# Performance work log

Measured on AMD Instinct MI355X. Metric: run time of the kernel, lower is better.

Reference implementation:

```python
import jax, jax.numpy as jnp
import numpy as np

H = 8          # num_heads
DK = 64        # head dim (head_size // num_heads)
SPARSITY = 0.5 # pre-softmax random drop probability
DROPOUT = 0.1  # post-softmax dropout probability


def setup_inputs() -> dict:
    key = jax.random.key(0)
    ks = jax.random.split(key, 12)
    B, S, D = 4, 2048, 512
    mk = lambda k, shp, scale=1.0: (jax.random.normal(k, shp, dtype=jnp.float32) * scale)
    return {
        "query": mk(ks[0], (B, S, D)),
        "key": mk(ks[1], (B, S, D)),
        "value": mk(ks[2], (B, S, D)),
        "Wq": mk(ks[3], (D, D), 0.04),
        "bq": mk(ks[4], (D,), 0.02),
        "Wk": mk(ks[5], (D, D), 0.04),
        "bk": mk(ks[6], (D,), 0.02),
        "Wv": mk(ks[7], (D, D), 0.04),
        "bv": mk(ks[8], (D,), 0.02),
        "Wo": mk(ks[9], (D, D), 0.04),
        "bo": mk(ks[10], (D,), 0.02),
    }


def _split_heads(x, B):
    # [B, S, H*DK] -> [B, H, S, DK]
    return x.reshape(B, -1, H, DK).transpose(0, 2, 1, 3)


def reference(query, key, value, Wq, bq, Wk, bk, Wv, bv, Wo, bo):
    B, S, D = query.shape
    # q/k/v projections (torch Linear: x @ W.T + b)
    q = _split_heads(query @ Wq.T + bq, B)   # [B, H, S, DK]
    k = _split_heads(key @ Wk.T + bk, B)
    v = _split_heads(value @ Wv.T + bv, B)

    scores = jnp.einsum("bhqd,bhkd->bhqk", q, k) / jnp.sqrt(jnp.float32(DK))

    # random pre-softmax sparsity mask: keep where U(0,1) > sparsity
    mkey = jax.random.fold_in(jax.random.key(42), 1)
    keep_sparse = jax.random.uniform(mkey, scores.shape) > SPARSITY
    scores = jnp.where(keep_sparse, scores, -jnp.inf)

    p_attn = jax.nn.softmax(scores, axis=-1)

    # dropout on attention probs, inverted scaling as in torch
    dkey = jax.random.fold_in(jax.random.key(42), 2)
    keep_drop = jax.random.uniform(dkey, p_attn.shape) >= DROPOUT
    p_attn = jnp.where(keep_drop, p_attn / (1.0 - DROPOUT), 0.0)

    x = jnp.einsum("bhqk,bhkd->bhqd", p_attn, v)        # [B, H, S, DK]
    x = x.transpose(0, 2, 1, 3).reshape(B, S, H * DK)    # [B, S, D]
    return x @ Wo.T + bo
```

## Files before the change

### kernel.cpp

```cpp
#include <hip/hip_runtime.h>
#include <stdint.h>

#define BATCH  4
#define SQ     2048
#define DMODEL 512
#define NH     8
#define DK     64

typedef __attribute__((ext_vector_type(8))) short short8;
typedef __attribute__((ext_vector_type(4))) float f32x4;

struct TFK { uint32_t a, b; };
constexpr uint32_t rotl_ce(uint32_t x, int d) {
  return (x << d) | (x >> (32 - d));
}
constexpr TFK tf_ce(uint32_t k0, uint32_t k1, uint32_t x0, uint32_t x1) {
  const uint32_t ks[3] = {k0, k1, k0 ^ k1 ^ 0x1BD11BDAu};
  const int rot[2][4] = {{13, 15, 26, 6}, {17, 29, 16, 24}};
  x0 += k0; x1 += k1;
  for (int c = 0; c < 5; ++c) {
    for (int j = 0; j < 4; ++j) {
      x0 += x1; x1 = rotl_ce(x1, rot[c & 1][j]); x1 ^= x0;
    }
    x0 += ks[(c + 1) % 3];
    x1 += ks[(c + 2) % 3] + (uint32_t)(c + 1);
  }
  return TFK{x0, x1};
}
constexpr TFK SPK = tf_ce(0u, 42u, 0u, 1u);
constexpr TFK DPK = tf_ce(0u, 42u, 0u, 2u);

#define SP_THR 0x80000200u
#define DP_THR 0x1999A200u

struct TfArgs {
  uint32_t sp[8];
  uint32_t dp[8];
  uint32_t sp_thr, dp_thr;
};

__device__ __forceinline__ void tf_round(uint32_t &x0, uint32_t &x1, int d) {
  x0 += x1;
  x1 = __builtin_amdgcn_alignbit(x1, x1, 32 - d);
  x1 ^= x0;
}
__device__ __forceinline__ void tf_grp(uint32_t &x0, uint32_t &x1,
                                       uint32_t injx1, uint32_t injx0, int d0,
                                       int d1, int d2, int d3) {
  x1 += injx1;
  x0 = x0 + injx0 + x1;
  x1 = __builtin_amdgcn_alignbit(x1, x1, 32 - d0);
  x1 ^= x0;
  tf_round(x0, x1, d1);
  tf_round(x0, x1, d2);
  tf_round(x0, x1, d3);
}
__device__ __forceinline__ uint32_t tf_rt(const uint32_t *__restrict__ c,
                                          uint32_t ctr) {
  uint32_t x1 = c[1] + ctr;
  uint32_t x0 = c[0] + x1;
  x1 = __builtin_amdgcn_alignbit(x1, x1, 19);
  x1 ^= x0;
  tf_round(x0, x1, 15);
  tf_round(x0, x1, 26);
  tf_round(x0, x1, 6);
  tf_grp(x0, x1, c[2], c[1], 17, 29, 16, 24);
  tf_grp(x0, x1, c[3], c[7], 13, 15, 26, 6);
  tf_grp(x0, x1, c[4], c[0], 17, 29, 16, 24);
  tf_grp(x0, x1, c[5], c[1], 13, 15, 26, 6);
  return (x0 + c[7]) ^ (x1 + c[6]);
}

__device__ __forceinline__ ushort f2bf_rne(float f) {
  uint32_t u = __float_as_uint(f);
  return (ushort)((u + 0x7fffu + ((u >> 16) & 1u)) >> 16);
}
__device__ __forceinline__ float bf2f(ushort h) {
  return __uint_as_float((uint32_t)h << 16);
}
__device__ __forceinline__ float exp_scaled(float s) {
#if __has_builtin(__builtin_amdgcn_exp2f)
  return __builtin_amdgcn_exp2f(s * 0.18033688011112042f);
#else
  return __expf(s * 0.125f);
#endif
}

__device__ __forceinline__ void split4(const float *__restrict__ src,
                                       ushort *__restrict__ dh,
                                       ushort *__restrict__ dl, size_t base) {
  float4 x = *(const float4 *)(src + base);
  uint32_t h[4], lo[4];
#pragma unroll
  for (int i = 0; i < 4; ++i) {
    float xi = ((const float *)&x)[i];
    ushort hh = f2bf_rne(xi);
    h[i] = hh;
    lo[i] = f2bf_rne(xi - bf2f(hh));
  }
  uint2 ph, pl;
  ph.x = h[0] | (h[1] << 16);  ph.y = h[2] | (h[3] << 16);
  pl.x = lo[0] | (lo[1] << 16); pl.y = lo[2] | (lo[3] << 16);
  *(uint2 *)(dh + base) = ph;
  *(uint2 *)(dl + base) = pl;
}

__global__ __launch_bounds__(256) void split_inputs_k(
    const float *__restrict__ q, const float *__restrict__ k,
    const float *__restrict__ v, ushort *__restrict__ qh,
    ushort *__restrict__ ql, ushort *__restrict__ kh, ushort *__restrict__ kl,
    ushort *__restrict__ vh, ushort *__restrict__ vl) {
  const float *src = blockIdx.y == 0 ? q : (blockIdx.y == 1 ? k : v);
  ushort *dh = blockIdx.y == 0 ? qh : (blockIdx.y == 1 ? kh : vh);
  ushort *dl = blockIdx.y == 0 ? ql : (blockIdx.y == 1 ? kl : vl);
  const size_t base = ((size_t)blockIdx.x * 256 + threadIdx.x) * 4;
  split4(src, dh, dl, base);
}

__global__ __launch_bounds__(256) void split_w_k(
    const float *__restrict__ w0, const float *__restrict__ w1,
    const float *__restrict__ w2, const float *__restrict__ w3,
    ushort *__restrict__ h0, ushort *__restrict__ l0, ushort *__restrict__ h1,
    ushort *__restrict__ l1, ushort *__restrict__ h2, ushort *__restrict__ l2,
    ushort *__restrict__ h3, ushort *__restrict__ l3) {
  const int y = blockIdx.y;
  const float *src = y == 0 ? w0 : (y == 1 ? w1 : (y == 2 ? w2 : w3));
  ushort *dh = y == 0 ? h0 : (y == 1 ? h1 : (y == 2 ? h2 : h3));
  ushort *dl = y == 0 ? l0 : (y == 1 ? l1 : (y == 2 ? l2 : l3));
  const size_t base = ((size_t)blockIdx.x * 256 + threadIdx.x) * 4;
  split4(src, dh, dl, base);
}

template <int MODE>
__global__ __launch_bounds__(256) void proj_mfma(
    const ushort *__restrict__ Ah, const ushort *__restrict__ Al,
    const ushort *__restrict__ Bh, const ushort *__restrict__ Bl,
    const float *__restrict__ bias, void *__restrict__ Yv) {
  __shared__ ushort Tt[MODE == 2 ? 128 * 72 : 1];
  const int tid = threadIdx.x;
  const int w = tid >> 6, l = tid & 63;
  const int lr = l & 15, lq = l >> 4;
  const int am = blockIdx.y * 128 + w * 32;
  const int bn = blockIdx.x * 64;
  f32x4 acc[2][4];
#pragma unroll
  for (int i = 0; i < 2; ++i)
#pragma unroll
    for (int j = 0; j < 4; ++j) acc[i][j] = (f32x4){0.f, 0.f, 0.f, 0.f};

#pragma unroll 2
  for (int k0 = 0; k0 < DMODEL; k0 += 32) {
    short8 ah[2], al[2], bh[4], bl[4];
#pragma unroll
    for (int mf = 0; mf < 2; ++mf) {
      const size_t off = (size_t)(am + mf * 16 + lr) * DMODEL + k0 + lq * 8;
      ah[mf] = *(const short8 *)(Ah + off);
      al[mf] = *(const short8 *)(Al + off);
    }
#pragma unroll
    for (int nf = 0; nf < 4; ++nf) {
      const size_t off = (size_t)(bn + nf * 16 + lr) * DMODEL + k0 + lq * 8;
      bh[nf] = *(const short8 *)(Bh + off);
      bl[nf] = *(const short8 *)(Bl + off);
    }
#pragma unroll
    for (int mf = 0; mf < 2; ++mf)
#pragma unroll
      for (int nf = 0; nf < 4; ++nf) {
        acc[mf][nf] = __builtin_amdgcn_mfma_f32_16x16x32_bf16(
            ah[mf], bh[nf], acc[mf][nf], 0, 0, 0);
        acc[mf][nf] = __builtin_amdgcn_mfma_f32_16x16x32_bf16(
            ah[mf], bl[nf], acc[mf][nf], 0, 0, 0);
        acc[mf][nf] = __builtin_amdgcn_mfma_f32_16x16x32_bf16(
            al[mf], bh[nf], acc[mf][nf], 0, 0, 0);
      }
  }

  if (MODE == 2) {
#pragma unroll
    for (int mf = 0; mf < 2; ++mf)
#pragma unroll
      for (int nf = 0; nf < 4; ++nf) {
        const int gn2 = am + mf * 16 + lq * 4;
#pragma unroll
        for (int r = 0; r < 4; ++r) {
          const int featl = (w * 32 + mf * 16 + lq * 4 + r);
          Tt[featl * 72 + nf * 16 + lr] =
              f2bf_rne(acc[mf][nf][r] + bias[gn2 + r]);
        }
      }
    __syncthreads();
    ushort *Y = (ushort *)Yv;
    const int feat = tid >> 1, half = tid & 1;
    const int gfeat = blockIdx.y * 128 + feat;
    const int bcol = bn >> 11, scol = (bn & 2047) + half * 32;
    ushort *dst = Y + ((size_t)(bcol * DMODEL + gfeat)) * SQ + scol;
    const ushort *srcp = &Tt[feat * 72 + half * 32];
#pragma unroll
    for (int j = 0; j < 4; ++j)
      *(uint4 *)(dst + j * 8) = *(const uint4 *)(srcp + j * 8);
    return;
  }

#pragma unroll
  for (int mf = 0; mf < 2; ++mf)
#pragma unroll
    for (int nf = 0; nf < 4; ++nf) {
      const int gn = bn + nf * 16 + lr;
      const float bb = bias[gn];
      if (MODE == 0) {
        float *Y = (float *)Yv;
#pragma unroll
        for (int r = 0; r < 4; ++r) {
          const int gm = am + mf * 16 + lq * 4 + r;
          Y[(size_t)gm * DMODEL + gn] = acc[mf][nf][r] + bb;
        }
      } else {
        ushort *Y = (ushort *)Yv;
#pragma unroll
        for (int r = 0; r < 4; ++r) {
          const int gm = am + mf * 16 + lq * 4 + r;
          Y[(size_t)gm * DMODEL + gn] = f2bf_rne(acc[mf][nf][r] + bb);
        }
      }
    }
}

__global__ __launch_bounds__(256, 2) void attn_mfma(
    const ushort *__restrict__ qp, const ushort *__restrict__ kp,
    const ushort *__restrict__ vpt, ushort *__restrict__ xah,
    ushort *__restrict__ xal, TfArgs ta) {
  __shared__ __align__(16) uint8_t lds[40960];
  const int b = blockIdx.z, h = blockIdx.y;
  const int qb = blockIdx.x * 64;
  const int tid = threadIdx.x;
  const int w = tid >> 6, l = tid & 63;
  const int lr = l & 15, lq = l >> 4;
  uint8_t *Ps = lds + 32768 + w * 2048;
  const int bh = b * NH + h;

  short8 qf[2];
  {
    const int qrow = qb + w * 16 + lr;
    const ushort *qrowp = qp + ((size_t)(b * SQ + qrow)) * DMODEL + h * DK;
    qf[0] = *(const short8 *)(qrowp + lq * 8);
    qf[1] = *(const short8 *)(qrowp + 32 + lq * 8);
  }
  f32x4 o[4];
  f32x4 lacc;
#pragma unroll
  for (int nd = 0; nd < 4; ++nd) o[nd] = (f32x4){0.f, 0.f, 0.f, 0.f};
  lacc = (f32x4){0.f, 0.f, 0.f, 0.f};

  uint32_t rowflat[4];
#pragma unroll
  for (int r = 0; r < 4; ++r)
    rowflat[r] = ((uint32_t)(bh * SQ + qb + w * 16 + lq * 4 + r)) << 11;

  const int srow = tid >> 2;
  const int sc0 = (tid & 3) * 2;
  const int ssw = (srow & 7) << 4;
  const ushort *kbase =
      kp + ((size_t)(b * SQ) + srow) * DMODEL + h * DK + sc0 * 8;
  const ushort *vbase = vpt + ((size_t)(bh * DK + srow)) * SQ + sc0 * 8;
  const int la0 = (srow * 128 + sc0 * 16) ^ ssw;
  const int la1 = (srow * 128 + (sc0 + 1) * 16) ^ ssw;

  uint4 kr0, kr1, vr0, vr1;
#define ISSUE(kv_)                                            \
  {                                                           \
    const ushort *ks_ = kbase + (size_t)(kv_)*DMODEL;         \
    kr0 = *(const uint4 *)ks_;                                \
    kr1 = *(const uint4 *)(ks_ + 8);                          \
    const ushort *vs_ = vbase + (kv_);                        \
    vr0 = *(const uint4 *)vs_;                                \
    vr1 = *(const uint4 *)(vs_ + 8);                          \
  }
#define STORE(buf_)                                           \
  {                                                           \
    uint8_t *Kb_ = lds + (buf_)*8192;                         \
    uint8_t *Vb_ = lds + 16384 + (buf_)*8192;                 \
    *(uint4 *)(Kb_ + la0) = kr0;                              \
    *(uint4 *)(Kb_ + la1) = kr1;                              \
    *(uint4 *)(Vb_ + la0) = vr0;                              \
    *(uint4 *)(Vb_ + la1) = vr1;                              \
  }

  ISSUE(0)
  STORE(0)
  __syncthreads();

  for (int kv = 0; kv < SQ; kv += 64) {
    const int cur = (kv >> 6) & 1;
    uint8_t *Ks = lds + cur * 8192;
    uint8_t *Vt = lds + 16384 + cur * 8192;
    const bool more = (kv + 64) < SQ;
    if (more) ISSUE(kv + 64)

    f32x4 s[4];
#pragma unroll
    for (int ni = 0; ni < 4; ++ni) s[ni] = (f32x4){0.f, 0.f, 0.f, 0.f};
#pragma unroll
    for (int ni = 0; ni < 4; ++ni) {
      const int krow = ni * 16 + lr;
      const int sw = (krow & 7) << 4;
#pragma unroll
      for (int kf = 0; kf < 2; ++kf) {
        short8 kb =
            *(const short8 *)(Ks + ((krow * 128 + kf * 64 + lq * 16) ^ sw));
        s[ni] =
            __builtin_amdgcn_mfma_f32_16x16x32_bf16(qf[kf], kb, s[ni], 0, 0, 0);
      }
    }

    const uint32_t colbase = (uint32_t)(kv + lr);
#pragma unroll
    for (int ni = 0; ni < 4; ++ni) {
#pragma unroll
      for (int r = 0; r < 4; ++r) {
        const uint32_t ctr = rowflat[r] + colbase + (uint32_t)(ni * 16);
        const bool keep_s = tf_rt(ta.sp, ctr) >= ta.sp_thr;
        const bool keep_d = tf_rt(ta.dp, ctr) >= ta.dp_thr;
        float e = exp_scaled(s[ni][r]);
        float p = keep_s ? e : 0.0f;
        lacc[r] += p;
        float pd = keep_d ? p * (1.0f / 0.9f) : 0.0f;
        const int prow = lq * 4 + r;
        *(ushort *)(Ps +
                    ((prow * 128 + (ni * 16 + lr) * 2) ^ ((prow & 7) << 4))) =
            f2bf_rne(pd);
      }
    }

#pragma unroll
    for (int kf = 0; kf < 2; ++kf) {
      short8 pa = *(const short8 *)(Ps + ((lr * 128 + kf * 64 + lq * 16) ^
                                          ((lr & 7) << 4)));
#pragma unroll
      for (int nd = 0; nd < 4; ++nd) {
        const int vrow = nd * 16 + lr;
        short8 vb = *(const short8 *)(Vt + ((vrow * 128 + kf * 64 + lq * 16) ^
                                            ((vrow & 7) << 4)));
        o[nd] = __builtin_amdgcn_mfma_f32_16x16x32_bf16(pa, vb, o[nd], 0, 0, 0);
      }
    }

    if (more) STORE(cur ^ 1)
    __syncthreads();
  }
#undef ISSUE
#undef STORE

  float inv[4];
#pragma unroll
  for (int r = 0; r < 4; ++r) {
    float t = lacc[r];
    t += __shfl_xor(t, 1);
    t += __shfl_xor(t, 2);
    t += __shfl_xor(t, 4);
    t += __shfl_xor(t, 8);
    inv[r] = 1.0f / t;
  }
#pragma unroll
  for (int nd = 0; nd < 4; ++nd)
#pragma unroll
    for (int r = 0; r < 4; ++r) {
      const int qrow = qb + w * 16 + lq * 4 + r;
      const size_t idx =
          ((size_t)(b * SQ + qrow)) * DMODEL + h * DK + nd * 16 + lr;
      const float val = o[nd][r] * inv[r];
      const ushort hh = f2bf_rne(val);
      xah[idx] = hh;
      xal[idx] = f2bf_rne(val - bf2f(hh));
    }
}

extern "C" void kernel_launch(void *const *d_in, const int *in_sizes, int n_in,
                              void *d_out, int out_size, void *d_ws,
                              size_t ws_size, hipStream_t stream) {
  (void)in_sizes; (void)n_in; (void)out_size;
  const float *query = (const float *)d_in[0];
  const float *key_  = (const float *)d_in[1];
  const float *value = (const float *)d_in[2];
  const float *Wq = (const float *)d_in[3];
  const float *bq = (const float *)d_in[4];
  const float *Wk = (const float *)d_in[5];
  const float *bk = (const float *)d_in[6];
  const float *Wv = (const float *)d_in[7];
  const float *bv = (const float *)d_in[8];
  const float *Wo = (const float *)d_in[9];
  const float *bo = (const float *)d_in[10];
  float *out = (float *)d_out;

  const size_t MB = (size_t)1 << 20;
  if (ws_size < 92 * MB) return;

  char *ws = (char *)d_ws;
  ushort *qih = (ushort *)(ws);
  ushort *qil = (ushort *)(ws + 8 * MB);
  ushort *kih = (ushort *)(ws + 16 * MB);
  ushort *kil = (ushort *)(ws + 24 * MB);
  ushort *vih = (ushort *)(ws + 32 * MB);
  ushort *vil = (ushort *)(ws + 40 * MB);
  ushort *Wqh = (ushort *)(ws + 48 * MB);
  ushort *Wql = (ushort *)(ws + 48 * MB + 512 * 1024);
  ushort *Wkh = (ushort *)(ws + 49 * MB);
  ushort *Wkl = (ushort *)(ws + 49 * MB + 512 * 1024);
  ushort *Wvh = (ushort *)(ws + 50 * MB);
  ushort *Wvl = (ushort *)(ws + 50 * MB + 512 * 1024);
  ushort *Woh = (ushort *)(ws + 51 * MB);
  ushort *Wol = (ushort *)(ws + 51 * MB + 512 * 1024);
  ushort *qp  = (ushort *)(ws + 52 * MB);
  ushort *kp  = (ushort *)(ws + 60 * MB);
  ushort *vpt = (ushort *)(ws + 68 * MB);
  ushort *xah = (ushort *)(ws + 76 * MB);
  ushort *xal = (ushort *)(ws + 84 * MB);

  constexpr uint32_t KS2s = SPK.a ^ SPK.b ^ 0x1BD11BDAu;
  constexpr uint32_t KS2d = DPK.a ^ DPK.b ^ 0x1BD11BDAu;
  TfArgs ta = {
      {SPK.a, SPK.b, KS2s + 1u, SPK.a + 2u, SPK.b + 3u, KS2s + 4u, SPK.a + 5u,
       KS2s},
      {DPK.a, DPK.b, KS2d + 1u, DPK.a + 2u, DPK.b + 3u, KS2d + 4u, DPK.a + 5u,
       KS2d},
      SP_THR, DP_THR};

  split_inputs_k<<<dim3(4096, 3), 256, 0, stream>>>(query, key_, value, qih,
                                                    qil, kih, kil, vih, vil);
  split_w_k<<<dim3(256, 4), 256, 0, stream>>>(Wq, Wk, Wv, Wo, Wqh, Wql, Wkh,
                                              Wkl, Wvh, Wvl, Woh, Wol);

  proj_mfma<1><<<dim3(8, 64), 256, 0, stream>>>(qih, qil, Wqh, Wql, bq, qp);
  proj_mfma<1><<<dim3(8, 64), 256, 0, stream>>>(kih, kil, Wkh, Wkl, bk, kp);
  proj_mfma<2><<<dim3(128, 4), 256, 0, stream>>>(Wvh, Wvl, vih, vil, bv, vpt);

  attn_mfma<<<dim3(SQ / 64, NH, BATCH), 256, 0, stream>>>(qp, kp, vpt, xah,
                                                          xal, ta);

  proj_mfma<0><<<dim3(8, 64), 256, 0, stream>>>(xah, xal, Woh, Wol, bo, out);
}
```

Measured before the change: 715.5 us.

## Precompute part of dropout/sparsity bitmasks in earlier memory-bound kernels

Moves Threefry mask generation for the last portion of attention rows (rows at or past ROW_CUT) into the split and projection kernels. Each thread there packs 32 keep bits for both masks into words stored in the workspace. Attention blocks past the cut then read two uint2 words per row instead of running the RNG per element. The goal is to hide ALU-heavy RNG work inside kernels bound by memory or MFMA. The cost is extra workspace, extra work in the earlier kernels, and an uneven split of work across attention blocks.

```diff
diff --git a/kernel.cpp b/kernel.cpp
--- a/kernel.cpp
+++ b/kernel.cpp
@@ -6,6 +6,10 @@
 #define DMODEL 512
 #define NH     8
 #define DK     64
+
+#define ROW_CUT   57344u
+#define W0        3670016u
+#define NPAIR     524288u
 
 typedef __attribute__((ext_vector_type(8))) short short8;
 typedef __attribute__((ext_vector_type(4))) float f32x4;
@@ -71,6 +75,21 @@
   return (x0 + c[7]) ^ (x1 + c[6]);
 }
 
+__device__ __forceinline__ void gen_mask_pair(uint32_t pairidx,
+                                              const TfArgs &ta,
+                                              uint32_t *__restrict__ spw,
+                                              uint32_t *__restrict__ dpw) {
+  const uint32_t base = (W0 + pairidx) << 5;
+  uint32_t sw = 0u, dw = 0u;
+#pragma unroll 4
+  for (uint32_t t = 0; t < 32; ++t) {
+    sw |= (tf_rt(ta.sp, base + t) >= ta.sp_thr ? 1u : 0u) << t;
+    dw |= (tf_rt(ta.dp, base + t) >= ta.dp_thr ? 1u : 0u) << t;
+  }
+  spw[pairidx] = sw;
+  dpw[pairidx] = dw;
+}
+
 __device__ __forceinline__ ushort f2bf_rne(float f) {
   uint32_t u = __float_as_uint(f);
   return (ushort)((u + 0x7fffu + ((u >> 16) & 1u)) >> 16);
@@ -109,12 +128,16 @@
     const float *__restrict__ q, const float *__restrict__ k,
     const float *__restrict__ v, ushort *__restrict__ qh,
     ushort *__restrict__ ql, ushort *__restrict__ kh, ushort *__restrict__ kl,
-    ushort *__restrict__ vh, ushort *__restrict__ vl) {
+    ushort *__restrict__ vh, ushort *__restrict__ vl,
+    uint32_t *__restrict__ spw, uint32_t *__restrict__ dpw, TfArgs ta) {
   const float *src = blockIdx.y == 0 ? q : (blockIdx.y == 1 ? k : v);
   ushort *dh = blockIdx.y == 0 ? qh : (blockIdx.y == 1 ? kh : vh);
   ushort *dl = blockIdx.y == 0 ? ql : (blockIdx.y == 1 ? kl : vl);
   const size_t base = ((size_t)blockIdx.x * 256 + threadIdx.x) * 4;
   split4(src, dh, dl, base);
+  const uint32_t flat =
+      (blockIdx.y * 4096u + blockIdx.x) * 256u + threadIdx.x;
+  if (flat < 131072u) gen_mask_pair(flat, ta, spw, dpw);
 }
 
 __global__ __launch_bounds__(256) void split_w_k(
@@ -122,20 +145,25 @@
     const float *__restrict__ w2, const float *__restrict__ w3,
     ushort *__restrict__ h0, ushort *__restrict__ l0, ushort *__restrict__ h1,
     ushort *__restrict__ l1, ushort *__restrict__ h2, ushort *__restrict__ l2,
-    ushort *__restrict__ h3, ushort *__restrict__ l3) {
+    ushort *__restrict__ h3, ushort *__restrict__ l3,
+    uint32_t *__restrict__ spw, uint32_t *__restrict__ dpw, TfArgs ta) {
   const int y = blockIdx.y;
   const float *src = y == 0 ? w0 : (y == 1 ? w1 : (y == 2 ? w2 : w3));
   ushort *dh = y == 0 ? h0 : (y == 1 ? h1 : (y == 2 ? h2 : h3));
   ushort *dl = y == 0 ? l0 : (y == 1 ? l1 : (y == 2 ? l2 : l3));
   const size_t base = ((size_t)blockIdx.x * 256 + threadIdx.x) * 4;
   split4(src, dh, dl, base);
+  const uint32_t flat = (blockIdx.y * 256u + blockIdx.x) * 256u + threadIdx.x;
+  if (flat < 32768u) gen_mask_pair(131072u + flat, ta, spw, dpw);
 }
 
 template <int MODE>
 __global__ __launch_bounds__(256) void proj_mfma(
     const ushort *__restrict__ Ah, const ushort *__restrict__ Al,
     const ushort *__restrict__ Bh, const ushort *__restrict__ Bl,
-    const float *__restrict__ bias, void *__restrict__ Yv) {
+    const float *__restrict__ bias, void *__restrict__ Yv,
+    uint32_t mbase, uint32_t mcount, uint32_t *__restrict__ spw,
+    uint32_t *__restrict__ dpw, TfArgs ta) {
   __shared__ ushort Tt[MODE == 2 ? 128 * 72 : 1];
   const int tid = threadIdx.x;
   const int w = tid >> 6, l = tid & 63;
@@ -199,37 +227,43 @@
 #pragma unroll
     for (int j = 0; j < 4; ++j)
       *(uint4 *)(dst + j * 8) = *(const uint4 *)(srcp + j * 8);
-    return;
-  }
-
-#pragma unroll
-  for (int mf = 0; mf < 2; ++mf)
-#pragma unroll
-    for (int nf = 0; nf < 4; ++nf) {
-      const int gn = bn + nf * 16 + lr;
-      const float bb = bias[gn];
-      if (MODE == 0) {
-        float *Y = (float *)Yv;
-#pragma unroll
-        for (int r = 0; r < 4; ++r) {
-          const int gm = am + mf * 16 + lq * 4 + r;
-          Y[(size_t)gm * DMODEL + gn] = acc[mf][nf][r] + bb;
+  } else {
+#pragma unroll
+    for (int mf = 0; mf < 2; ++mf)
+#pragma unroll
+      for (int nf = 0; nf < 4; ++nf) {
+        const int gn = bn + nf * 16 + lr;
+        const float bb = bias[gn];
+        if (MODE == 0) {
+          float *Y = (float *)Yv;
+#pragma unroll
+          for (int r = 0; r < 4; ++r) {
+            const int gm = am + mf * 16 + lq * 4 + r;
+            Y[(size_t)gm * DMODEL + gn] = acc[mf][nf][r] + bb;
+          }
+        } else {
+          ushort *Y = (ushort *)Yv;
+#pragma unroll
+          for (int r = 0; r < 4; ++r) {
+            const int gm = am + mf * 16 + lq * 4 + r;
+            Y[(size_t)gm * DMODEL + gn] = f2bf_rne(acc[mf][nf][r] + bb);
+          }
         }
-      } else {
-        ushort *Y = (ushort *)Yv;
-#pragma unroll
-        for (int r = 0; r < 4; ++r) {
-          const int gm = am + mf * 16 + lq * 4 + r;
-          Y[(size_t)gm * DMODEL + gn] = f2bf_rne(acc[mf][nf][r] + bb);
-        }
-      }
-    }
+      }
+  }
+
+  if (mcount) {
+    const uint32_t flat =
+        (blockIdx.y * gridDim.x + blockIdx.x) * 256u + threadIdx.x;
+    if (flat < mcount) gen_mask_pair(mbase + flat, ta, spw, dpw);
+  }
 }
 
 __global__ __launch_bounds__(256, 2) void attn_mfma(
     const ushort *__restrict__ qp, const ushort *__restrict__ kp,
     const ushort *__restrict__ vpt, ushort *__restrict__ xah,
-    ushort *__restrict__ xal, TfArgs ta) {
+    ushort *__restrict__ xal, const uint32_t *__restrict__ spw,
+    const uint32_t *__restrict__ dpw, TfArgs ta) {
   __shared__ __align__(16) uint8_t lds[40960];
   const int b = blockIdx.z, h = blockIdx.y;
   const int qb = blockIdx.x * 64;
@@ -238,6 +272,7 @@
   const int lr = l & 15, lq = l >> 4;
   uint8_t *Ps = lds + 32768 + w * 2048;
   const int bh = b * NH + h;
+  const bool use_pre = (uint32_t)(bh * SQ + qb) >= ROW_CUT;
 
   short8 qf[2];
   {
@@ -252,10 +287,13 @@
   for (int nd = 0; nd < 4; ++nd) o[nd] = (f32x4){0.f, 0.f, 0.f, 0.f};
   lacc = (f32x4){0.f, 0.f, 0.f, 0.f};
 
-  uint32_t rowflat[4];
-#pragma unroll
-  for (int r = 0; r < 4; ++r)
-    rowflat[r] = ((uint32_t)(bh * SQ + qb + w * 16 + lq * 4 + r)) << 11;
+  uint32_t rowflat[4], rowcomp[4];
+#pragma unroll
+  for (int r = 0; r < 4; ++r) {
+    const uint32_t rowidx = (uint32_t)(bh * SQ + qb + w * 16 + lq * 4 + r);
+    rowflat[r] = rowidx << 11;
+    rowcomp[r] = (rowidx - ROW_CUT) * 64u;
+  }
 
   const int srow = tid >> 2;
   const int sc0 = (tid & 3) * 2;
@@ -313,22 +351,45 @@
       }
     }
 
-    const uint32_t colbase = (uint32_t)(kv + lr);
-#pragma unroll
-    for (int ni = 0; ni < 4; ++ni) {
+    auto process = [&](int ni, int r, bool keep_s, bool keep_d) {
+      float e = exp_scaled(s[ni][r]);
+      float p = keep_s ? e : 0.0f;
+      lacc[r] += p;
+      float pd = keep_d ? p * (1.0f / 0.9f) : 0.0f;
+      const int prow = lq * 4 + r;
+      *(ushort *)(Ps +
+                  ((prow * 128 + (ni * 16 + lr) * 2) ^ ((prow & 7) << 4))) =
+          f2bf_rne(pd);
+    };
+
+    if (!use_pre) {
+      const uint32_t colbase = (uint32_t)(kv + lr);
+#pragma unroll
+      for (int ni = 0; ni < 4; ++ni) {
+#pragma unroll
+        for (int r = 0; r < 4; ++r) {
+          const uint32_t ctr = rowflat[r] + colbase + (uint32_t)(ni * 16);
+          process(ni, r, tf_rt(ta.sp, ctr) >= ta.sp_thr,
+                  tf_rt(ta.dp, ctr) >= ta.dp_thr);
+        }
+      }
+    } else {
+      uint2 swd[4], dwd[4];
 #pragma unroll
       for (int r = 0; r < 4; ++r) {
-        const uint32_t ctr = rowflat[r] + colbase + (uint32_t)(ni * 16);
-        const bool keep_s = tf_rt(ta.sp, ctr) >= ta.sp_thr;
-        const bool keep_d = tf_rt(ta.dp, ctr) >= ta.dp_thr;
-        float e = exp_scaled(s[ni][r]);
-        float p = keep_s ? e : 0.0f;
-        lacc[r] += p;
-        float pd = keep_d ? p * (1.0f / 0.9f) : 0.0f;
-        const int prow = lq * 4 + r;
-        *(ushort *)(Ps +
-                    ((prow * 128 + (ni * 16 + lr) * 2) ^ ((prow & 7) << 4))) =
-            f2bf_rne(pd);
+        const uint32_t wb = rowcomp[r] + (uint32_t)(kv >> 5);
+        swd[r] = *(const uint2 *)(spw + wb);
+        dwd[r] = *(const uint2 *)(dpw + wb);
+      }
+#pragma unroll
+      for (int ni = 0; ni < 4; ++ni) {
+        const int bpos = (ni & 1) * 16 + lr;
+#pragma unroll
+        for (int r = 0; r < 4; ++r) {
+          const uint32_t sws = (ni < 2) ? swd[r].x : swd[r].y;
+          const uint32_t dws = (ni < 2) ? dwd[r].x : dwd[r].y;
+          process(ni, r, (sws >> bpos) & 1u, (dws >> bpos) & 1u);
+        }
       }
     }
 
@@ -393,7 +454,7 @@
   float *out = (float *)d_out;
 
   const size_t MB = (size_t)1 << 20;
-  if (ws_size < 92 * MB) return;
+  if (ws_size < 96 * MB) return;
 
   char *ws = (char *)d_ws;
   ushort *qih = (ushort *)(ws);
@@ -415,6 +476,8 @@
   ushort *vpt = (ushort *)(ws + 68 * MB);
   ushort *xah = (ushort *)(ws + 76 * MB);
   ushort *xal = (ushort *)(ws + 84 * MB);
+  uint32_t *spw = (uint32_t *)(ws + 92 * MB);
+  uint32_t *dpw = (uint32_t *)(ws + 94 * MB);
 
   constexpr uint32_t KS2s = SPK.a ^ SPK.b ^ 0x1BD11BDAu;
   constexpr uint32_t KS2d = DPK.a ^ DPK.b ^ 0x1BD11BDAu;
@@ -425,17 +488,22 @@
        KS2d},
       SP_THR, DP_THR};
 
-  split_inputs_k<<<dim3(4096, 3), 256, 0, stream>>>(query, key_, value, qih,
-                                                    qil, kih, kil, vih, vil);
+  split_inputs_k<<<dim3(4096, 3), 256, 0, stream>>>(
+      query, key_, value, qih, qil, kih, kil, vih, vil, spw, dpw, ta);
   split_w_k<<<dim3(256, 4), 256, 0, stream>>>(Wq, Wk, Wv, Wo, Wqh, Wql, Wkh,
-                                              Wkl, Wvh, Wvl, Woh, Wol);
-
-  proj_mfma<1><<<dim3(8, 64), 256, 0, stream>>>(qih, qil, Wqh, Wql, bq, qp);
-  proj_mfma<1><<<dim3(8, 64), 256, 0, stream>>>(kih, kil, Wkh, Wkl, bk, kp);
-  proj_mfma<2><<<dim3(128, 4), 256, 0, stream>>>(Wvh, Wvl, vih, vil, bv, vpt);
+                                              Wkl, Wvh, Wvl, Woh, Wol, spw,
+                                              dpw, ta);
+
+  proj_mfma<1><<<dim3(8, 64), 256, 0, stream>>>(qih, qil, Wqh, Wql, bq, qp,
+                                                163840u, 131072u, spw, dpw, ta);
+  proj_mfma<1><<<dim3(8, 64), 256, 0, stream>>>(kih, kil, Wkh, Wkl, bk, kp,
+                                                294912u, 131072u, spw, dpw, ta);
+  proj_mfma<2><<<dim3(128, 4), 256, 0, stream>>>(Wvh, Wvl, vih, vil, bv, vpt,
+                                                 425984u, 98304u, spw, dpw, ta);
 
   attn_mfma<<<dim3(SQ / 64, NH, BATCH), 256, 0, stream>>>(qp, kp, vpt, xah,
-                                                          xal, ta);
-
-  proj_mfma<0><<<dim3(8, 64), 256, 0, stream>>>(xah, xal, Woh, Wol, bo, out);
-}
+                                                          xal, spw, dpw, ta);
+
+  proj_mfma<0><<<dim3(8, 64), 256, 0, stream>>>(xah, xal, Woh, Wol, bo, out, 0u,
+                                                0u, spw, dpw, ta);
+}
```

Result: slower. 784.5 us (+9.6%).

## Fuse fp32-to-bf16 split of query/key into projection GEMM and merge split kernels

Applied to the files above, without the earlier changes.

The Q and K projections now read fp32 activations directly and do the hi/lo bf16 split in registers. This removes the separate split pass and its 16 MB-per-tensor scratch writes and reads. The remaining value and weight splits are merged into one launch, the Q and K projections share one launch, and the output projection uses a new tiling of one 16-row fragment per wave with wider N. The trade-off is that A-side split work is recomputed for each N tile, and the loop is not unrolled, which may reduce latency hiding.

```diff
diff --git a/kernel.cpp b/kernel.cpp
--- a/kernel.cpp
+++ b/kernel.cpp
@@ -105,38 +105,126 @@
   *(uint2 *)(dl + base) = pl;
 }
 
-__global__ __launch_bounds__(256) void split_inputs_k(
+__global__ __launch_bounds__(256) void split_all(
+    const float *__restrict__ value, const float *__restrict__ Wq,
+    const float *__restrict__ Wk, const float *__restrict__ Wv,
+    const float *__restrict__ Wo, ushort *__restrict__ vh,
+    ushort *__restrict__ vl, ushort *__restrict__ Wqh,
+    ushort *__restrict__ Wql, ushort *__restrict__ Wkh,
+    ushort *__restrict__ Wkl, ushort *__restrict__ Wvh,
+    ushort *__restrict__ Wvl, ushort *__restrict__ Woh,
+    ushort *__restrict__ Wol) {
+  const int bid = blockIdx.x;
+  const float *src;
+  ushort *dh, *dl;
+  uint32_t lb;
+  if (bid < 4096) {
+    src = value; dh = vh; dl = vl; lb = bid;
+  } else {
+    const int t = bid - 4096;
+    const int wsel = t >> 8;
+    lb = t & 255;
+    src = wsel == 0 ? Wq : (wsel == 1 ? Wk : (wsel == 2 ? Wv : Wo));
+    dh = wsel == 0 ? Wqh : (wsel == 1 ? Wkh : (wsel == 2 ? Wvh : Woh));
+    dl = wsel == 0 ? Wql : (wsel == 1 ? Wkl : (wsel == 2 ? Wvl : Wol));
+  }
+  const size_t base = ((size_t)lb * 256 + threadIdx.x) * 4;
+  split4(src, dh, dl, base);
+}
+
+template <int NF, bool ASPL, bool FOUT>
+__device__ __forceinline__ void proj_body(
+    const float *__restrict__ Af, const ushort *__restrict__ Ah,
+    const ushort *__restrict__ Al, const ushort *__restrict__ Bh,
+    const ushort *__restrict__ Bl, const float *__restrict__ bias,
+    void *__restrict__ Yv, int am, int bn, int lr, int lq) {
+  f32x4 acc[NF];
+#pragma unroll
+  for (int nf = 0; nf < NF; ++nf) acc[nf] = (f32x4){0.f, 0.f, 0.f, 0.f};
+  const int arow = am + lr;
+
+#pragma unroll 1
+  for (int k0 = 0; k0 < DMODEL; k0 += 32) {
+    short8 ah, al;
+    if (ASPL) {
+      const float *ap = Af + (size_t)arow * DMODEL + k0 + lq * 8;
+      float4 x0 = *(const float4 *)ap;
+      float4 x1 = *(const float4 *)(ap + 4);
+      float xs[8] = {x0.x, x0.y, x0.z, x0.w, x1.x, x1.y, x1.z, x1.w};
+#pragma unroll
+      for (int i = 0; i < 8; ++i) {
+        const ushort hh = f2bf_rne(xs[i]);
+        ((ushort *)&ah)[i] = hh;
+        ((ushort *)&al)[i] = f2bf_rne(xs[i] - bf2f(hh));
+      }
+    } else {
+      const size_t off = (size_t)arow * DMODEL + k0 + lq * 8;
+      ah = *(const short8 *)(Ah + off);
+      al = *(const short8 *)(Al + off);
+    }
+#pragma unroll
+    for (int nf = 0; nf < NF; ++nf) {
+      const size_t off = (size_t)(bn + nf * 16 + lr) * DMODEL + k0 + lq * 8;
+      short8 bh = *(const short8 *)(Bh + off);
+      short8 bl = *(const short8 *)(Bl + off);
+      acc[nf] = __builtin_amdgcn_mfma_f32_16x16x32_bf16(ah, bh, acc[nf], 0, 0, 0);
+      acc[nf] = __builtin_amdgcn_mfma_f32_16x16x32_bf16(ah, bl, acc[nf], 0, 0, 0);
+      acc[nf] = __builtin_amdgcn_mfma_f32_16x16x32_bf16(al, bh, acc[nf], 0, 0, 0);
+    }
+  }
+
+#pragma unroll
+  for (int nf = 0; nf < NF; ++nf) {
+    const int gn = bn + nf * 16 + lr;
+    const float bb = bias[gn];
+#pragma unroll
+    for (int r = 0; r < 4; ++r) {
+      const int gm = am + lq * 4 + r;
+      if (FOUT)
+        ((float *)Yv)[(size_t)gm * DMODEL + gn] = acc[nf][r] + bb;
+      else
+        ((ushort *)Yv)[(size_t)gm * DMODEL + gn] = f2bf_rne(acc[nf][r] + bb);
+    }
+  }
+}
+
+__global__ __launch_bounds__(256) void proj_qk(
     const float *__restrict__ q, const float *__restrict__ k,
-    const float *__restrict__ v, ushort *__restrict__ qh,
-    ushort *__restrict__ ql, ushort *__restrict__ kh, ushort *__restrict__ kl,
-    ushort *__restrict__ vh, ushort *__restrict__ vl) {
-  const float *src = blockIdx.y == 0 ? q : (blockIdx.y == 1 ? k : v);
-  ushort *dh = blockIdx.y == 0 ? qh : (blockIdx.y == 1 ? kh : vh);
-  ushort *dl = blockIdx.y == 0 ? ql : (blockIdx.y == 1 ? kl : vl);
-  const size_t base = ((size_t)blockIdx.x * 256 + threadIdx.x) * 4;
-  split4(src, dh, dl, base);
-}
-
-__global__ __launch_bounds__(256) void split_w_k(
-    const float *__restrict__ w0, const float *__restrict__ w1,
-    const float *__restrict__ w2, const float *__restrict__ w3,
-    ushort *__restrict__ h0, ushort *__restrict__ l0, ushort *__restrict__ h1,
-    ushort *__restrict__ l1, ushort *__restrict__ h2, ushort *__restrict__ l2,
-    ushort *__restrict__ h3, ushort *__restrict__ l3) {
-  const int y = blockIdx.y;
-  const float *src = y == 0 ? w0 : (y == 1 ? w1 : (y == 2 ? w2 : w3));
-  ushort *dh = y == 0 ? h0 : (y == 1 ? h1 : (y == 2 ? h2 : h3));
-  ushort *dl = y == 0 ? l0 : (y == 1 ? l1 : (y == 2 ? l2 : l3));
-  const size_t base = ((size_t)blockIdx.x * 256 + threadIdx.x) * 4;
-  split4(src, dh, dl, base);
-}
-
-template <int MODE>
-__global__ __launch_bounds__(256) void proj_mfma(
+    const ushort *__restrict__ Wqh, const ushort *__restrict__ Wql,
+    const ushort *__restrict__ Wkh, const ushort *__restrict__ Wkl,
+    const float *__restrict__ bq, const float *__restrict__ bk,
+    ushort *__restrict__ qp, ushort *__restrict__ kp) {
+  const int tid = threadIdx.x;
+  const int w = tid >> 6, l = tid & 63;
+  const int lr = l & 15, lq = l >> 4;
+  const int am = blockIdx.y * 64 + w * 16;
+  const int bn = blockIdx.x * 256;
+  if (blockIdx.z == 0)
+    proj_body<16, true, false>(q, nullptr, nullptr, Wqh, Wql, bq, qp, am, bn,
+                               lr, lq);
+  else
+    proj_body<16, true, false>(k, nullptr, nullptr, Wkh, Wkl, bk, kp, am, bn,
+                               lr, lq);
+}
+
+__global__ __launch_bounds__(256) void proj_out(
+    const ushort *__restrict__ xah, const ushort *__restrict__ xal,
+    const ushort *__restrict__ Woh, const ushort *__restrict__ Wol,
+    const float *__restrict__ bo, float *__restrict__ out) {
+  const int tid = threadIdx.x;
+  const int w = tid >> 6, l = tid & 63;
+  const int lr = l & 15, lq = l >> 4;
+  const int am = blockIdx.y * 64 + w * 16;
+  const int bn = blockIdx.x * 128;
+  proj_body<8, false, true>(nullptr, xah, xal, Woh, Wol, bo, out, am, bn, lr,
+                            lq);
+}
+
+__global__ __launch_bounds__(256) void proj_vt(
     const ushort *__restrict__ Ah, const ushort *__restrict__ Al,
     const ushort *__restrict__ Bh, const ushort *__restrict__ Bl,
-    const float *__restrict__ bias, void *__restrict__ Yv) {
-  __shared__ ushort Tt[MODE == 2 ? 128 * 72 : 1];
+    const float *__restrict__ bias, ushort *__restrict__ Y) {
+  __shared__ ushort Tt[128 * 72];
   const int tid = threadIdx.x;
   const int w = tid >> 6, l = tid & 63;
   const int lr = l & 15, lq = l >> 4;
@@ -176,54 +264,27 @@
       }
   }
 
-  if (MODE == 2) {
-#pragma unroll
-    for (int mf = 0; mf < 2; ++mf)
-#pragma unroll
-      for (int nf = 0; nf < 4; ++nf) {
-        const int gn2 = am + mf * 16 + lq * 4;
-#pragma unroll
-        for (int r = 0; r < 4; ++r) {
-          const int featl = (w * 32 + mf * 16 + lq * 4 + r);
-          Tt[featl * 72 + nf * 16 + lr] =
-              f2bf_rne(acc[mf][nf][r] + bias[gn2 + r]);
-        }
-      }
-    __syncthreads();
-    ushort *Y = (ushort *)Yv;
-    const int feat = tid >> 1, half = tid & 1;
-    const int gfeat = blockIdx.y * 128 + feat;
-    const int bcol = bn >> 11, scol = (bn & 2047) + half * 32;
-    ushort *dst = Y + ((size_t)(bcol * DMODEL + gfeat)) * SQ + scol;
-    const ushort *srcp = &Tt[feat * 72 + half * 32];
-#pragma unroll
-    for (int j = 0; j < 4; ++j)
-      *(uint4 *)(dst + j * 8) = *(const uint4 *)(srcp + j * 8);
-    return;
-  }
-
 #pragma unroll
   for (int mf = 0; mf < 2; ++mf)
 #pragma unroll
     for (int nf = 0; nf < 4; ++nf) {
-      const int gn = bn + nf * 16 + lr;
-      const float bb = bias[gn];
-      if (MODE == 0) {
-        float *Y = (float *)Yv;
-#pragma unroll
-        for (int r = 0; r < 4; ++r) {
-          const int gm = am + mf * 16 + lq * 4 + r;
-          Y[(size_t)gm * DMODEL + gn] = acc[mf][nf][r] + bb;
-        }
-      } else {
-        ushort *Y = (ushort *)Yv;
-#pragma unroll
-        for (int r = 0; r < 4; ++r) {
-          const int gm = am + mf * 16 + lq * 4 + r;
-          Y[(size_t)gm * DMODEL + gn] = f2bf_rne(acc[mf][nf][r] + bb);
-        }
-      }
-    }
+      const int gn2 = am + mf * 16 + lq * 4;
+#pragma unroll
+      for (int r = 0; r < 4; ++r) {
+        const int featl = (w * 32 + mf * 16 + lq * 4 + r);
+        Tt[featl * 72 + nf * 16 + lr] =
+            f2bf_rne(acc[mf][nf][r] + bias[gn2 + r]);
+      }
+    }
+  __syncthreads();
+  const int feat = tid >> 1, half = tid & 1;
+  const int gfeat = blockIdx.y * 128 + feat;
+  const int bcol = bn >> 11, scol = (bn & 2047) + half * 32;
+  ushort *dst = Y + ((size_t)(bcol * DMODEL + gfeat)) * SQ + scol;
+  const ushort *srcp = &Tt[feat * 72 + half * 32];
+#pragma unroll
+  for (int j = 0; j < 4; ++j)
+    *(uint4 *)(dst + j * 8) = *(const uint4 *)(srcp + j * 8);
 }
 
 __global__ __launch_bounds__(256, 2) void attn_mfma(
@@ -393,28 +454,24 @@
   float *out = (float *)d_out;
 
   const size_t MB = (size_t)1 << 20;
-  if (ws_size < 92 * MB) return;
+  if (ws_size < 60 * MB) return;
 
   char *ws = (char *)d_ws;
-  ushort *qih = (ushort *)(ws);
-  ushort *qil = (ushort *)(ws + 8 * MB);
-  ushort *kih = (ushort *)(ws + 16 * MB);
-  ushort *kil = (ushort *)(ws + 24 * MB);
-  ushort *vih = (ushort *)(ws + 32 * MB);
-  ushort *vil = (ushort *)(ws + 40 * MB);
-  ushort *Wqh = (ushort *)(ws + 48 * MB);
-  ushort *Wql = (ushort *)(ws + 48 * MB + 512 * 1024);
-  ushort *Wkh = (ushort *)(ws + 49 * MB);
-  ushort *Wkl = (ushort *)(ws + 49 * MB + 512 * 1024);
-  ushort *Wvh = (ushort *)(ws + 50 * MB);
-  ushort *Wvl = (ushort *)(ws + 50 * MB + 512 * 1024);
-  ushort *Woh = (ushort *)(ws + 51 * MB);
-  ushort *Wol = (ushort *)(ws + 51 * MB + 512 * 1024);
-  ushort *qp  = (ushort *)(ws + 52 * MB);
-  ushort *kp  = (ushort *)(ws + 60 * MB);
-  ushort *vpt = (ushort *)(ws + 68 * MB);
-  ushort *xah = (ushort *)(ws + 76 * MB);
-  ushort *xal = (ushort *)(ws + 84 * MB);
+  ushort *vih = (ushort *)(ws);
+  ushort *vil = (ushort *)(ws + 8 * MB);
+  ushort *Wqh = (ushort *)(ws + 16 * MB);
+  ushort *Wql = (ushort *)(ws + 16 * MB + 512 * 1024);
+  ushort *Wkh = (ushort *)(ws + 17 * MB);
+  ushort *Wkl = (ushort *)(ws + 17 * MB + 512 * 1024);
+  ushort *Wvh = (ushort *)(ws + 18 * MB);
+  ushort *Wvl = (ushort *)(ws + 18 * MB + 512 * 1024);
+  ushort *Woh = (ushort *)(ws + 19 * MB);
+  ushort *Wol = (ushort *)(ws + 19 * MB + 512 * 1024);
+  ushort *qp  = (ushort *)(ws + 20 * MB);
+  ushort *kp  = (ushort *)(ws + 28 * MB);
+  ushort *vpt = (ushort *)(ws + 36 * MB);
+  ushort *xah = (ushort *)(ws + 44 * MB);
+  ushort *xal = (ushort *)(ws + 52 * MB);
 
   constexpr uint32_t KS2s = SPK.a ^ SPK.b ^ 0x1BD11BDAu;
   constexpr uint32_t KS2d = DPK.a ^ DPK.b ^ 0x1BD11BDAu;
@@ -425,17 +482,16 @@
        KS2d},
       SP_THR, DP_THR};
 
-  split_inputs_k<<<dim3(4096, 3), 256, 0, stream>>>(query, key_, value, qih,
-                                                    qil, kih, kil, vih, vil);
-  split_w_k<<<dim3(256, 4), 256, 0, stream>>>(Wq, Wk, Wv, Wo, Wqh, Wql, Wkh,
-                                              Wkl, Wvh, Wvl, Woh, Wol);
-
-  proj_mfma<1><<<dim3(8, 64), 256, 0, stream>>>(qih, qil, Wqh, Wql, bq, qp);
-  proj_mfma<1><<<dim3(8, 64), 256, 0, stream>>>(kih, kil, Wkh, Wkl, bk, kp);
-  proj_mfma<2><<<dim3(128, 4), 256, 0, stream>>>(Wvh, Wvl, vih, vil, bv, vpt);
+  split_all<<<5120, 256, 0, stream>>>(value, Wq, Wk, Wv, Wo, vih, vil, Wqh,
+                                      Wql, Wkh, Wkl, Wvh, Wvl, Woh, Wol);
+
+  proj_qk<<<dim3(2, 128, 2), 256, 0, stream>>>(query, key_, Wqh, Wql, Wkh, Wkl,
+                                               bq, bk, qp, kp);
+
+  proj_vt<<<dim3(128, 4), 256, 0, stream>>>(Wvh, Wvl, vih, vil, bv, vpt);
 
   attn_mfma<<<dim3(SQ / 64, NH, BATCH), 256, 0, stream>>>(qp, kp, vpt, xah,
                                                           xal, ta);
 
-  proj_mfma<0><<<dim3(8, 64), 256, 0, stream>>>(xah, xal, Woh, Wol, bo, out);
-}
+  proj_out<<<dim3(4, 128), 256, 0, stream>>>(xah, xal, Woh, Wol, bo, out);
+}
```

Result: slower. 758.0 us (+5.9%).
